# Kernel tuning notes

Hardware: AMD Instinct MI355X
Metric: run time of the kernel (lower is better)

Reference implementation:

```python
import jax, jax.numpy as jnp
import numpy as np

D = 128  # dim_input / kernel_num
S = 1    # support_num
NL, NM, NG = 5, 20, 100

def _norm(x, axis):
    return x / jnp.maximum(jnp.linalg.norm(x, axis=axis, keepdims=True), 1e-12)

def _gather(t, idx):
    # t: (b,n,c), idx: (b,n,k) -> (b,n,k,c)
    return jax.vmap(lambda tb, ib: tb[ib])(t, idx)

def _knn(v, k):
    sq = jnp.sum(v * v, axis=-1)
    d = sq[:, :, None] + sq[:, None, :] - 2.0 * jnp.einsum('bic,bjc->bij', v, v)
    _, idx = jax.lax.top_k(-d, k + 1)
    return idx[:, :, 1:]  # drop self

def _conv_surface(idx, v, dirs):
    nd = _norm(_gather(v, idx) - v[:, :, None, :], -1)                    # (b,n,k,3)
    theta = jax.nn.relu(jnp.einsum('bnkc,cd->bnkd', nd, _norm(dirs, 0)))  # (b,n,k,S*D)
    b, n, k, _ = theta.shape
    theta = theta.reshape(b, n, k, S, D)
    return jnp.sum(jnp.max(theta, axis=2), axis=2)                         # (b,n,D)

def _conv_layer(idx, v, fm, W, bias, dirs):
    nd = _norm(_gather(v, idx) - v[:, :, None, :], -1)
    theta = jax.nn.relu(jnp.einsum('bnkc,cd->bnkd', nd, _norm(dirs, 0)))  # (b,n,k,S*D)
    fo = fm @ W + bias                                                    # (b,n,(S+1)*D)
    fc, fs = fo[..., :D], fo[..., D:]
    fs = _gather(fs, idx)                                                 # (b,n,k,S*D)
    b, n, k, _ = theta.shape
    act = (theta * fs).reshape(b, n, k, S, D)
    return fc + jnp.sum(jnp.max(act, axis=2), axis=2)                     # (b,n,D)

def _bn_relu(x, g, b, eps=1e-5):
    # training-mode BatchNorm1d over (batch, points) per channel, then ReLU
    m = jnp.mean(x, axis=(0, 1))
    v = jnp.var(x, axis=(0, 1))
    return jax.nn.relu((x - m) * jax.lax.rsqrt(v + eps) * g + b)

def setup_inputs() -> dict:
    key = jax.random.key(0)
    ks = jax.random.split(key, 16)
    B, N = 4, 1024
    def u(k, shape, fan):
        s = 1.0 / np.sqrt(fan)
        return jax.random.uniform(k, shape, jnp.float32, -s, s)
    inp = {}
    inp['vertices'] = jax.random.normal(ks[0], (B, N, 3), jnp.float32)
    inp['dirs_l'] = u(ks[1], (3, S * D), S * D)
    inp['dirs_m0'] = u(ks[2], (3, S * D), S * D)
    inp['W_m1'] = u(ks[3], (D, (S + 1) * D), (S + 1) * D)
    inp['b_m1'] = u(ks[4], ((S + 1) * D,), (S + 1) * D)
    inp['dirs_m1'] = u(ks[5], (3, S * D), S * D)
    inp['dirs_g0'] = u(ks[6], (3, S * D), S * D)
    inp['W_g1'] = u(ks[7], (D, (S + 1) * D), (S + 1) * D)
    inp['b_g1'] = u(ks[8], ((S + 1) * D,), (S + 1) * D)
    inp['dirs_g1'] = u(ks[9], (3, S * D), S * D)
    inp['W_g2'] = u(ks[10], (D, (S + 1) * D), (S + 1) * D)
    inp['b_g2'] = u(ks[11], ((S + 1) * D,), (S + 1) * D)
    inp['dirs_g2'] = u(ks[12], (3, S * D), S * D)
    for nm in ['l', 'm0', 'm1', 'g0', 'g1', 'g2']:
        inp['g_' + nm] = jnp.ones((D,), jnp.float32)
        inp['be_' + nm] = jnp.zeros((D,), jnp.float32)
    inp['W_down'] = u(ks[13], (3 * D, 2 * D), 3 * D)
    inp['b_down'] = u(ks[14], (2 * D,), 3 * D)
    return inp

def reference(vertices, dirs_l, dirs_m0, W_m1, b_m1, dirs_m1, dirs_g0, W_g1, b_g1, dirs_g1, W_g2, b_g2, dirs_g2, g_l, be_l, g_m0, be_m0, g_m1, be_m1, g_g0, be_g0, g_g1, be_g1, g_g2, be_g2, W_down, b_down):
    il = _knn(vertices, NL)
    im = _knn(vertices, NM)
    ig = _knn(vertices, NG)
    fm_l = _bn_relu(_conv_surface(il, vertices, dirs_l), g_l, be_l)
    fm_m = _bn_relu(_conv_surface(im, vertices, dirs_m0), g_m0, be_m0)
    fm_m = _bn_relu(_conv_layer(im, vertices, fm_m, W_m1, b_m1, dirs_m1), g_m1, be_m1)
    fm_g = _bn_relu(_conv_surface(ig, vertices, dirs_g0), g_g0, be_g0)
    fm_g = _bn_relu(_conv_layer(ig, vertices, fm_g, W_g1, b_g1, dirs_g1), g_g1, be_g1)
    fm_g = _bn_relu(_conv_layer(ig, vertices, fm_g, W_g2, b_g2, dirs_g2), g_g2, be_g2)
    out = jnp.concatenate((fm_l, fm_m, fm_g), axis=2)                      # (b,n,3D)
    return jax.nn.relu(out @ W_down + b_down)                              # (b,n,2D)
```

## Files before the change

### kernel.cpp

```cpp
#include <hip/hip_runtime.h>
#include <math.h>

typedef unsigned long long u64;

__global__ __launch_bounds__(256) void knnsurf_kernel(
    const float* __restrict__ verts,
    int* __restrict__ idx_out, float4* __restrict__ nd_out,
    const float* __restrict__ dl, const float* __restrict__ dm,
    const float* __restrict__ dg,
    float* __restrict__ raw_l, float* __restrict__ raw_m, float* __restrict__ raw_g)
{
    __shared__ float4 vps[1024];
    __shared__ __align__(16) u64 cand[4][208];
    const int tid = threadIdx.x;
    const int row0 = blockIdx.x * 4;
    const int b = row0 >> 10;
    const float* vb = verts + b * 3072;

    for (int n = tid; n < 1024; n += 256) {
        float x = vb[3 * n], y = vb[3 * n + 1], z = vb[3 * n + 2];
        float s = __fadd_rn(__fadd_rn(__fmul_rn(x, x), __fmul_rn(y, y)),
                            __fmul_rn(z, z));
        vps[n] = make_float4(x, y, z, s);
    }
    __syncthreads();

    const int w = tid >> 6, lane = tid & 63;
    const int row = row0 + w;
    const int n_i = row & 1023;
    const float4 pi = vps[n_i];
    const float xi = pi.x, yi = pi.y, zi = pi.z, sqi = pi.w;

    u64 K[16];
    u64 m1 = ~0ULL, m2 = ~0ULL;
#pragma unroll
    for (int t = 0; t < 16; ++t) {
        int j = t * 64 + lane;
        float4 p = vps[j];
        float dot = __fadd_rn(__fadd_rn(__fmul_rn(xi, p.x),
                                        __fmul_rn(yi, p.y)),
                              __fmul_rn(zi, p.z));
        float d = __fsub_rn(__fadd_rn(sqi, p.w), __fmul_rn(2.0f, dot));
        d = __fadd_rn(d, 0.0f);
        unsigned u = __float_as_uint(d);
        unsigned m = (u & 0x80000000u) ? ~u : (u | 0x80000000u);
        u64 k = ((u64)m << 10) | (unsigned)j;
        K[t] = k;
        bool lt1 = k < m1;
        u64 nm2 = lt1 ? m1 : ((k < m2) ? k : m2);
        m1 = lt1 ? k : m1;
        m2 = nm2;
    }

    u64 tmax = m2, tmin = m1;
#pragma unroll
    for (int off = 1; off < 64; off <<= 1) {
        u64 a = __shfl_xor(tmax, off); if (a > tmax) tmax = a;
        u64 c = __shfl_xor(tmin, off); if (c < tmin) tmin = c;
    }

    u64 T = tmax;
    int chi;
    {
        int c = 0;
#pragma unroll
        for (int t = 0; t < 16; ++t) c += (K[t] < T) ? 1 : 0;
#pragma unroll
        for (int off = 1; off < 64; off <<= 1) c += __shfl_xor(c, off);
        chi = c;
    }
    u64 lo = tmin, hi = T;
    while (chi > 192) {
        u64 mid = (lo + hi) >> 1;
        int c = 0;
#pragma unroll
        for (int t = 0; t < 16; ++t) c += (K[t] < mid) ? 1 : 0;
#pragma unroll
        for (int off = 1; off < 64; off <<= 1) c += __shfl_xor(c, off);
        if (c >= 101) { hi = mid; chi = c; } else lo = mid;
    }
    T = hi;
    const int n = chi;

    int myc_n = 0;
#pragma unroll
    for (int t = 0; t < 16; ++t) myc_n += (K[t] < T) ? 1 : 0;
    int sc = myc_n;
#pragma unroll
    for (int off = 1; off < 64; off <<= 1) {
        int v = __shfl_up(sc, off);
        if (lane >= off) sc += v;
    }
    int pos = sc - myc_n;
#pragma unroll
    for (int t = 0; t < 16; ++t) {
        if (K[t] < T) cand[w][pos++] = K[t];
    }
    if (lane == 0) cand[w][n] = ~0ULL;
    __syncthreads();

    u64 myc[3]; int rk[3];
#pragma unroll
    for (int q = 0; q < 3; ++q) {
        int i = lane + q * 64;
        myc[q] = (i < n) ? cand[w][i] : ~0ULL;
        rk[q] = 0;
    }
    {
        const ulonglong2* c2 = (const ulonglong2*)&cand[w][0];
        const int half = (n + 1) >> 1;
        for (int jj = 0; jj < half; ++jj) {
            ulonglong2 kk = c2[jj];
#pragma unroll
            for (int q = 0; q < 3; ++q) {
                rk[q] += (kk.x < myc[q]) ? 1 : 0;
                rk[q] += (kk.y < myc[q]) ? 1 : 0;
            }
        }
    }

    const int rowbase = row & ~1023;
    float4* nd4w = (float4*)&cand[w][0];
#pragma unroll
    for (int q = 0; q < 3; ++q) {
        int i = lane + q * 64;
        if (i < n) {
            int r = rk[q];
            if (r >= 1 && r <= 100) {
                int slot = r - 1;
                unsigned j = (unsigned)(myc[q] & 1023u);
                idx_out[row * 100 + slot] = rowbase + (int)j;
                float4 pj = vps[j];
                float dx = pj.x - xi, dy = pj.y - yi, dz = pj.z - zi;
                float nrm = sqrtf(__fadd_rn(__fadd_rn(__fmul_rn(dx, dx),
                                                      __fmul_rn(dy, dy)),
                                            __fmul_rn(dz, dz)));
                float inv = 1.0f / fmaxf(nrm, 1e-12f);
                float4 nv = make_float4(dx * inv, dy * inv, dz * inv, 0.0f);
                nd_out[row * 100 + slot] = nv;
                nd4w[slot] = nv;
            }
        }
    }
    __syncthreads();

    const int d = tid & 127;
    float lx = dl[d], ly = dl[128 + d], lz = dl[256 + d];
    float li = 1.0f / fmaxf(sqrtf((lx * lx + ly * ly) + lz * lz), 1e-12f);
    lx *= li; ly *= li; lz *= li;
    float mx = dm[d], my = dm[128 + d], mz = dm[256 + d];
    float mi = 1.0f / fmaxf(sqrtf((mx * mx + my * my) + mz * mz), 1e-12f);
    mx *= mi; my *= mi; mz *= mi;
    float gx = dg[d], gy = dg[128 + d], gz = dg[256 + d];
    float gi = 1.0f / fmaxf(sqrtf((gx * gx + gy * gy) + gz * gz), 1e-12f);
    gx *= gi; gy *= gi; gz *= gi;

#pragma unroll
    for (int p = 0; p < 2; ++p) {
        int rr = (tid >> 7) + 2 * p;
        const float4* ns = (const float4*)&cand[rr][0];
        float ml = -1e30f, mm = -1e30f, mg = -1e30f;
        int k = 0;
        for (; k < 5; ++k) {
            float4 v = ns[k];
            ml = fmaxf(ml, (v.x * lx + v.y * ly) + v.z * lz);
            mm = fmaxf(mm, (v.x * mx + v.y * my) + v.z * mz);
            mg = fmaxf(mg, (v.x * gx + v.y * gy) + v.z * gz);
        }
        for (; k < 20; ++k) {
            float4 v = ns[k];
            mm = fmaxf(mm, (v.x * mx + v.y * my) + v.z * mz);
            mg = fmaxf(mg, (v.x * gx + v.y * gy) + v.z * gz);
        }
        for (; k < 100; ++k) {
            float4 v = ns[k];
            mg = fmaxf(mg, (v.x * gx + v.y * gy) + v.z * gz);
        }
        int orow = row0 + rr;
        raw_l[orow * 128 + d] = fmaxf(ml, 0.0f);
        raw_m[orow * 128 + d] = fmaxf(mm, 0.0f);
        raw_g[orow * 128 + d] = fmaxf(mg, 0.0f);
    }
}

__global__ __launch_bounds__(256) void bnsum_kernel(
    const float* s0, double* p0,
    const float* s1, double* p1,
    const float* s2, double* p2)
{
    const int t = blockIdx.x >> 6;
    const int blk = blockIdx.x & 63;
    const float* src = (t == 0) ? s0 : (t == 1) ? s1 : s2;
    double* p = (t == 0) ? p0 : (t == 1) ? p1 : p2;
    const int tid = threadIdx.x;
    const int c = tid & 127, seg = tid >> 7;
    const float* q = src + ((size_t)blk * 64 + seg * 32) * 128 + c;
    double s = 0.0, ss = 0.0;
    for (int r = 0; r < 32; ++r) { float v = q[r * 128]; s += v; ss += (double)v * v; }
    __shared__ double Ls[2][128], Lq[2][128];
    Ls[seg][c] = s; Lq[seg][c] = ss;
    __syncthreads();
    if (tid < 128) {
        p[blk * 256 + c]       = Ls[0][c] + Ls[1][c];
        p[blk * 256 + 128 + c] = Lq[0][c] + Lq[1][c];
    }
}

__device__ __forceinline__ void compute_st(const double* __restrict__ p,
                                           const float* __restrict__ g,
                                           const float* __restrict__ e,
                                           float* stA, float* stB,
                                           int tid, int nthreads)
{
    for (int c = tid; c < 128; c += nthreads) {
        double S = 0.0, Q = 0.0;
#pragma unroll
        for (int bb = 0; bb < 64; ++bb) { S += p[bb * 256 + c]; Q += p[bb * 256 + 128 + c]; }
        double m = S * (1.0 / 4096.0);
        double var = Q * (1.0 / 4096.0) - m * m;
        double a = (double)g[c] / sqrt(var + 1e-5);
        stA[c] = (float)a;
        stB[c] = (float)((double)e[c] - m * a);
    }
}

__global__ __launch_bounds__(256) void gemm2_kernel(
    const float* __restrict__ Aa, const double* __restrict__ pa,
    const float* __restrict__ ga, const float* __restrict__ ea,
    const float* __restrict__ Wa, const float* __restrict__ ba, float* __restrict__ outa,
    const float* __restrict__ Ab, const double* __restrict__ pb,
    const float* __restrict__ gb, const float* __restrict__ eb,
    const float* __restrict__ Wb, const float* __restrict__ bb, float* __restrict__ outb)
{
    const int job = blockIdx.y;
    const float* A = job ? Ab : Aa;  const double* p = job ? pb : pa;
    const float* g = job ? gb : ga;  const float* e = job ? eb : ea;
    const float* W = job ? Wb : Wa;  const float* bias = job ? bb : ba;
    float* out = job ? outb : outa;

    __shared__ float stA[128], stB[128];
    __shared__ float As[8 * 128];
    const int o = threadIdx.x;
    const int r0 = blockIdx.x * 8;

    compute_st(p, g, e, stA, stB, o, 256);
    __syncthreads();

    for (int t = o; t < 8 * 128; t += 256) {
        int r = t >> 7, c = t & 127;
        As[t] = fmaxf(fmaf(stA[c], A[(r0 + r) * 128 + c], stB[c]), 0.0f);
    }
    __syncthreads();

    float acc[8];
    const float bz = bias[o];
#pragma unroll
    for (int r = 0; r < 8; ++r) acc[r] = bz;

    for (int c = 0; c < 128; c += 4) {
        float w0 = W[(c + 0) * 256 + o];
        float w1 = W[(c + 1) * 256 + o];
        float w2 = W[(c + 2) * 256 + o];
        float w3 = W[(c + 3) * 256 + o];
#pragma unroll
        for (int r = 0; r < 8; ++r) {
            const float4 av = *(const float4*)&As[r * 128 + c];
            acc[r] += av.x * w0 + av.y * w1 + av.z * w2 + av.w * w3;
        }
    }
#pragma unroll
    for (int r = 0; r < 8; ++r)
        out[(r0 + r) * 256 + o] = acc[r];
}

__global__ __launch_bounds__(128) void layer_kernel(
    const float4* __restrict__ nd, const int* __restrict__ idxbuf,
    const float* dir0, const float* fo0, float* out0, int K0,
    const float* dir1, const float* fo1, float* out1, int K1)
{
    const int job = blockIdx.y;
    const float* dirs = job ? dir1 : dir0;
    const float* fo = job ? fo1 : fo0;
    float* out = job ? out1 : out0;
    const int K = job ? K1 : K0;

    const int d = threadIdx.x;
    const int row = blockIdx.x;

    float dx = dirs[d], dy = dirs[128 + d], dz = dirs[256 + d];
    float di = 1.0f / fmaxf(sqrtf((dx * dx + dy * dy) + dz * dz), 1e-12f);
    dx *= di; dy *= di; dz *= di;

    const float4* ns = nd + (size_t)row * 100;
    const int* ib = idxbuf + (size_t)row * 100;

    float acc = -1e30f;
    for (int k4 = 0; k4 < K; k4 += 4) {
        int4 ix4 = *(const int4*)&ib[k4];
        float fs0 = fo[(size_t)ix4.x * 256 + 128 + d];
        float fs1 = fo[(size_t)ix4.y * 256 + 128 + d];
        float fs2 = fo[(size_t)ix4.z * 256 + 128 + d];
        float fs3 = fo[(size_t)ix4.w * 256 + 128 + d];
        float4 v0 = ns[k4 + 0];
        float4 v1 = ns[k4 + 1];
        float4 v2 = ns[k4 + 2];
        float4 v3 = ns[k4 + 3];
        float t0 = fmaxf((v0.x * dx + v0.y * dy) + v0.z * dz, 0.0f);
        float t1 = fmaxf((v1.x * dx + v1.y * dy) + v1.z * dz, 0.0f);
        float t2 = fmaxf((v2.x * dx + v2.y * dy) + v2.z * dz, 0.0f);
        float t3 = fmaxf((v3.x * dx + v3.y * dy) + v3.z * dz, 0.0f);
        acc = fmaxf(acc, t0 * fs0);
        acc = fmaxf(acc, t1 * fs1);
        acc = fmaxf(acc, t2 * fs2);
        acc = fmaxf(acc, t3 * fs3);
    }
    out[row * 128 + d] = fo[row * 256 + d] + acc;
}

__global__ __launch_bounds__(256) void gemmf_kernel(
    const float* __restrict__ A0, const double* __restrict__ p0,
    const float* __restrict__ g0, const float* __restrict__ e0,
    const float* __restrict__ A1, const double* __restrict__ p1,
    const float* __restrict__ g1, const float* __restrict__ e1,
    const float* __restrict__ A2, const double* __restrict__ p2,
    const float* __restrict__ g2, const float* __restrict__ e2,
    const float* __restrict__ W, const float* __restrict__ bias, float* __restrict__ out)
{
    __shared__ float stA[384], stB[384];
    __shared__ float As[8 * 384];
    const int o = threadIdx.x;
    const int r0 = blockIdx.x * 8;

    compute_st(p0, g0, e0, stA,       stB,       o, 256);
    compute_st(p1, g1, e1, stA + 128, stB + 128, o, 256);
    compute_st(p2, g2, e2, stA + 256, stB + 256, o, 256);
    __syncthreads();

    for (int t = o; t < 8 * 384; t += 256) {
        int r = t / 384, c = t - r * 384;
        int seg = c >> 7, cc = c & 127;
        const float* A = (seg == 0) ? A0 : (seg == 1) ? A1 : A2;
        As[t] = fmaxf(fmaf(stA[c], A[(r0 + r) * 128 + cc], stB[c]), 0.0f);
    }
    __syncthreads();

    float acc[8];
    const float bz = bias[o];
#pragma unroll
    for (int r = 0; r < 8; ++r) acc[r] = bz;

    for (int c = 0; c < 384; c += 4) {
        float w0 = W[(c + 0) * 256 + o];
        float w1 = W[(c + 1) * 256 + o];
        float w2 = W[(c + 2) * 256 + o];
        float w3 = W[(c + 3) * 256 + o];
#pragma unroll
        for (int r = 0; r < 8; ++r) {
            const float4 av = *(const float4*)&As[r * 384 + c];
            acc[r] += av.x * w0 + av.y * w1 + av.z * w2 + av.w * w3;
        }
    }
#pragma unroll
    for (int r = 0; r < 8; ++r)
        out[(r0 + r) * 256 + o] = fmaxf(acc[r], 0.0f);
}

extern "C" void kernel_launch(void* const* d_in, const int* in_sizes, int n_in,
                              void* d_out, int out_size, void* d_ws, size_t ws_size,
                              hipStream_t stream)
{
    (void)in_sizes; (void)n_in; (void)out_size; (void)ws_size;

    const float* verts   = (const float*)d_in[0];
    const float* dirs_l  = (const float*)d_in[1];
    const float* dirs_m0 = (const float*)d_in[2];
    const float* W_m1    = (const float*)d_in[3];
    const float* b_m1    = (const float*)d_in[4];
    const float* dirs_m1 = (const float*)d_in[5];
    const float* dirs_g0 = (const float*)d_in[6];
    const float* W_g1    = (const float*)d_in[7];
    const float* b_g1    = (const float*)d_in[8];
    const float* dirs_g1 = (const float*)d_in[9];
    const float* W_g2    = (const float*)d_in[10];
    const float* b_g2    = (const float*)d_in[11];
    const float* dirs_g2 = (const float*)d_in[12];
    const float* g_l  = (const float*)d_in[13]; const float* be_l  = (const float*)d_in[14];
    const float* g_m0 = (const float*)d_in[15]; const float* be_m0 = (const float*)d_in[16];
    const float* g_m1 = (const float*)d_in[17]; const float* be_m1 = (const float*)d_in[18];
    const float* g_g0 = (const float*)d_in[19]; const float* be_g0 = (const float*)d_in[20];
    const float* g_g1 = (const float*)d_in[21]; const float* be_g1 = (const float*)d_in[22];
    const float* g_g2 = (const float*)d_in[23]; const float* be_g2 = (const float*)d_in[24];
    const float* W_down = (const float*)d_in[25];
    const float* b_down = (const float*)d_in[26];

    char* ws = (char*)d_ws;
    const size_t MB = 1 << 20;
    int*    idx100 = (int*)   (ws + 0);
    double* p_l    = (double*)(ws + 2 * MB);
    double* p_m0   = p_l  + 32768;
    double* p_m1   = p_m0 + 32768;
    double* p_g0   = p_m1 + 32768;
    double* p_g1   = p_g0 + 32768;
    double* p_g2   = p_g1 + 32768;
    float4* nd100  = (float4*)(ws + 4 * MB);
    float* raw_l  = (float*)(ws + 11 * MB);
    float* raw_m0 = (float*)(ws + 13 * MB);
    float* raw_g0 = (float*)(ws + 15 * MB);
    float* raw_m1 = (float*)(ws + 17 * MB);
    float* raw_g1 = (float*)(ws + 19 * MB);
    float* raw_g2 = (float*)(ws + 21 * MB);
    float* fo_m   = (float*)(ws + 23 * MB);
    float* fo_g   = (float*)(ws + 27 * MB);
    float* fo_g2  = (float*)(ws + 31 * MB);

    knnsurf_kernel<<<1024, 256, 0, stream>>>(verts, idx100, nd100,
                                             dirs_l, dirs_m0, dirs_g0,
                                             raw_l, raw_m0, raw_g0);
    bnsum_kernel<<<192, 256, 0, stream>>>(raw_l, p_l, raw_m0, p_m0, raw_g0, p_g0);
    gemm2_kernel<<<dim3(512, 2), 256, 0, stream>>>(
        raw_m0, p_m0, g_m0, be_m0, W_m1, b_m1, fo_m,
        raw_g0, p_g0, g_g0, be_g0, W_g1, b_g1, fo_g);
    layer_kernel<<<dim3(4096, 2), 128, 0, stream>>>(nd100, idx100,
                                                    dirs_m1, fo_m, raw_m1, 20,
                                                    dirs_g1, fo_g, raw_g1, 100);
    bnsum_kernel<<<128, 256, 0, stream>>>(raw_m1, p_m1, raw_g1, p_g1, raw_g1, p_g1);
    gemm2_kernel<<<dim3(512, 1), 256, 0, stream>>>(
        raw_g1, p_g1, g_g1, be_g1, W_g2, b_g2, fo_g2,
        raw_g1, p_g1, g_g1, be_g1, W_g2, b_g2, fo_g2);
    layer_kernel<<<dim3(4096, 1), 128, 0, stream>>>(nd100, idx100,
                                                    dirs_g2, fo_g2, raw_g2, 100,
                                                    dirs_g2, fo_g2, raw_g2, 100);
    bnsum_kernel<<<64, 256, 0, stream>>>(raw_g2, p_g2, raw_g2, p_g2, raw_g2, p_g2);
    gemmf_kernel<<<512, 256, 0, stream>>>(raw_l, p_l, g_l, be_l,
                                          raw_m1, p_m1, g_m1, be_m1,
                                          raw_g2, p_g2, g_g2, be_g2,
                                          W_down, b_down, (float*)d_out);
}
```

Baseline: 273.0 us.

## Run dense GEMMs on bf16 MFMA with split-precision hi/lo emulation of fp32

The three dense matmul stages (gemm2 twice, gemmf) move from scalar FP32 FMA loops to MFMA 16x16x32 bf16 instructions. Three products (hi*hi, lo*hi, hi*lo) approximate fp32 accuracy. Weights are pre-split into hi/lo bf16 pairs and reordered into MFMA fragment layout at the tail of the knn kernel, and activations are split the same way into padded LDS. Tiles become 16 rows by 128 columns per block. This targets the ALU cost of the GEMMs, at the price of three MFMAs per tile, some precision loss from the dropped lo*lo term, and extra conversion work in the knn kernel.

```diff
diff --git a/kernel.cpp b/kernel.cpp
--- a/kernel.cpp
+++ b/kernel.cpp
@@ -2,13 +2,54 @@
 #include <math.h>
 
 typedef unsigned long long u64;
+typedef __attribute__((ext_vector_type(8))) short bfrag;
+typedef __attribute__((ext_vector_type(4))) float ffrag;
+
+__device__ __forceinline__ unsigned splitpack(float x)
+{
+    unsigned u = __float_as_uint(x);
+    unsigned hi = u >> 16;
+    float r = x - __uint_as_float(hi << 16);
+    unsigned v = __float_as_uint(r);
+    unsigned lo = (v + 0x7FFFu + ((v >> 16) & 1u)) >> 16;
+    return hi | (lo << 16);
+}
+
+__device__ void conv_wfrag(const float* __restrict__ W, unsigned* __restrict__ dst,
+                           int KB, int gid, int stride)
+{
+    int total = KB * 32 * 256;
+    for (int f = gid; f < total; f += stride) {
+        int i = f & 7;
+        int l = (f >> 3) & 63;
+        int t = f >> 9;
+        int kb = t % KB, ct = t / KB;
+        int k = kb * 32 + (l >> 4) * 8 + i;
+        int n = ct * 16 + (l & 15);
+        dst[f] = splitpack(W[k * 256 + n]);
+    }
+}
+
+#define UNPK8(H, L, q0, q1)                                                         \
+    H[0] = (short)(q0.x); L[0] = (short)(q0.x >> 16);                               \
+    H[1] = (short)(q0.y); L[1] = (short)(q0.y >> 16);                               \
+    H[2] = (short)(q0.z); L[2] = (short)(q0.z >> 16);                               \
+    H[3] = (short)(q0.w); L[3] = (short)(q0.w >> 16);                               \
+    H[4] = (short)(q1.x); L[4] = (short)(q1.x >> 16);                               \
+    H[5] = (short)(q1.y); L[5] = (short)(q1.y >> 16);                               \
+    H[6] = (short)(q1.z); L[6] = (short)(q1.z >> 16);                               \
+    H[7] = (short)(q1.w); L[7] = (short)(q1.w >> 16);
 
 __global__ __launch_bounds__(256) void knnsurf_kernel(
     const float* __restrict__ verts,
     int* __restrict__ idx_out, float4* __restrict__ nd_out,
     const float* __restrict__ dl, const float* __restrict__ dm,
     const float* __restrict__ dg,
-    float* __restrict__ raw_l, float* __restrict__ raw_m, float* __restrict__ raw_g)
+    float* __restrict__ raw_l, float* __restrict__ raw_m, float* __restrict__ raw_g,
+    const float* __restrict__ Wm1, const float* __restrict__ Wg1,
+    const float* __restrict__ Wg2, const float* __restrict__ Wdn,
+    unsigned* __restrict__ wf_m1, unsigned* __restrict__ wf_g1,
+    unsigned* __restrict__ wf_g2, unsigned* __restrict__ wf_dn)
 {
     __shared__ float4 vps[1024];
     __shared__ __align__(16) u64 cand[4][208];
@@ -181,6 +222,14 @@
         raw_m[orow * 128 + d] = fmaxf(mm, 0.0f);
         raw_g[orow * 128 + d] = fmaxf(mg, 0.0f);
     }
+
+    {
+        const int gid = blockIdx.x * 256 + tid;
+        conv_wfrag(Wm1, wf_m1, 4, gid, 262144);
+        conv_wfrag(Wg1, wf_g1, 4, gid, 262144);
+        conv_wfrag(Wg2, wf_g2, 4, gid, 262144);
+        conv_wfrag(Wdn, wf_dn, 12, gid, 262144);
+    }
 }
 
 __global__ __launch_bounds__(256) void bnsum_kernel(
@@ -227,50 +276,71 @@
 __global__ __launch_bounds__(256) void gemm2_kernel(
     const float* __restrict__ Aa, const double* __restrict__ pa,
     const float* __restrict__ ga, const float* __restrict__ ea,
-    const float* __restrict__ Wa, const float* __restrict__ ba, float* __restrict__ outa,
+    const unsigned* __restrict__ Wfa, const float* __restrict__ ba, float* __restrict__ outa,
     const float* __restrict__ Ab, const double* __restrict__ pb,
     const float* __restrict__ gb, const float* __restrict__ eb,
-    const float* __restrict__ Wb, const float* __restrict__ bb, float* __restrict__ outb)
-{
-    const int job = blockIdx.y;
+    const unsigned* __restrict__ Wfb, const float* __restrict__ bb, float* __restrict__ outb)
+{
+    const int job = blockIdx.z;
     const float* A = job ? Ab : Aa;  const double* p = job ? pb : pa;
     const float* g = job ? gb : ga;  const float* e = job ? eb : ea;
-    const float* W = job ? Wb : Wa;  const float* bias = job ? bb : ba;
+    const unsigned* Wf = job ? Wfb : Wfa;
+    const float* bias = job ? bb : ba;
     float* out = job ? outb : outa;
 
     __shared__ float stA[128], stB[128];
-    __shared__ float As[8 * 128];
-    const int o = threadIdx.x;
-    const int r0 = blockIdx.x * 8;
-
-    compute_st(p, g, e, stA, stB, o, 256);
-    __syncthreads();
-
-    for (int t = o; t < 8 * 128; t += 256) {
+    __shared__ __align__(16) unsigned Al[16 * 132];
+    const int tid = threadIdx.x;
+    const int r0 = blockIdx.x * 16;
+
+    compute_st(p, g, e, stA, stB, tid, 256);
+    __syncthreads();
+
+    for (int t = tid; t < 16 * 128; t += 256) {
         int r = t >> 7, c = t & 127;
-        As[t] = fmaxf(fmaf(stA[c], A[(r0 + r) * 128 + c], stB[c]), 0.0f);
-    }
-    __syncthreads();
-
-    float acc[8];
-    const float bz = bias[o];
-#pragma unroll
-    for (int r = 0; r < 8; ++r) acc[r] = bz;
-
-    for (int c = 0; c < 128; c += 4) {
-        float w0 = W[(c + 0) * 256 + o];
-        float w1 = W[(c + 1) * 256 + o];
-        float w2 = W[(c + 2) * 256 + o];
-        float w3 = W[(c + 3) * 256 + o];
-#pragma unroll
-        for (int r = 0; r < 8; ++r) {
-            const float4 av = *(const float4*)&As[r * 128 + c];
-            acc[r] += av.x * w0 + av.y * w1 + av.z * w2 + av.w * w3;
-        }
-    }
-#pragma unroll
-    for (int r = 0; r < 8; ++r)
-        out[(r0 + r) * 256 + o] = acc[r];
+        float v = fmaxf(fmaf(stA[c], A[(size_t)(r0 + r) * 128 + c], stB[c]), 0.0f);
+        Al[r * 132 + c] = splitpack(v);
+    }
+    __syncthreads();
+
+    const int lane = tid & 63, wv = tid >> 6;
+    const int ct0 = blockIdx.y * 8 + wv * 2;
+    const int col0 = ct0 * 16 + (lane & 15);
+    const float bz0 = bias[col0], bz1 = bias[col0 + 16];
+    ffrag acc0 = {bz0, bz0, bz0, bz0};
+    ffrag acc1 = {bz1, bz1, bz1, bz1};
+
+    const unsigned* ap0 = Al + (lane & 15) * 132 + (lane >> 4) * 8;
+
+#pragma unroll
+    for (int kb = 0; kb < 4; ++kb) {
+        const uint4* ap = (const uint4*)(ap0 + kb * 32);
+        uint4 aq0 = ap[0], aq1 = ap[1];
+        bfrag ah, al; UNPK8(ah, al, aq0, aq1)
+        {
+            const uint4* bp = (const uint4*)(Wf + ((size_t)(ct0 * 4 + kb) * 64 + lane) * 8);
+            uint4 bq0 = bp[0], bq1 = bp[1];
+            bfrag bh, bl; UNPK8(bh, bl, bq0, bq1)
+            acc0 = __builtin_amdgcn_mfma_f32_16x16x32_bf16(ah, bh, acc0, 0, 0, 0);
+            acc0 = __builtin_amdgcn_mfma_f32_16x16x32_bf16(al, bh, acc0, 0, 0, 0);
+            acc0 = __builtin_amdgcn_mfma_f32_16x16x32_bf16(ah, bl, acc0, 0, 0, 0);
+        }
+        {
+            const uint4* bp = (const uint4*)(Wf + ((size_t)((ct0 + 1) * 4 + kb) * 64 + lane) * 8);
+            uint4 bq0 = bp[0], bq1 = bp[1];
+            bfrag bh, bl; UNPK8(bh, bl, bq0, bq1)
+            acc1 = __builtin_amdgcn_mfma_f32_16x16x32_bf16(ah, bh, acc1, 0, 0, 0);
+            acc1 = __builtin_amdgcn_mfma_f32_16x16x32_bf16(al, bh, acc1, 0, 0, 0);
+            acc1 = __builtin_amdgcn_mfma_f32_16x16x32_bf16(ah, bl, acc1, 0, 0, 0);
+        }
+    }
+
+    const int rowb = r0 + (lane >> 4) * 4;
+#pragma unroll
+    for (int j = 0; j < 4; ++j) {
+        out[(size_t)(rowb + j) * 256 + col0]      = acc0[j];
+        out[(size_t)(rowb + j) * 256 + col0 + 16] = acc1[j];
+    }
 }
 
 __global__ __launch_bounds__(128) void layer_kernel(
@@ -324,45 +394,66 @@
     const float* __restrict__ g1, const float* __restrict__ e1,
     const float* __restrict__ A2, const double* __restrict__ p2,
     const float* __restrict__ g2, const float* __restrict__ e2,
-    const float* __restrict__ W, const float* __restrict__ bias, float* __restrict__ out)
+    const unsigned* __restrict__ Wf, const float* __restrict__ bias,
+    float* __restrict__ out)
 {
     __shared__ float stA[384], stB[384];
-    __shared__ float As[8 * 384];
-    const int o = threadIdx.x;
-    const int r0 = blockIdx.x * 8;
-
-    compute_st(p0, g0, e0, stA,       stB,       o, 256);
-    compute_st(p1, g1, e1, stA + 128, stB + 128, o, 256);
-    compute_st(p2, g2, e2, stA + 256, stB + 256, o, 256);
-    __syncthreads();
-
-    for (int t = o; t < 8 * 384; t += 256) {
+    __shared__ __align__(16) unsigned Al[16 * 388];
+    const int tid = threadIdx.x;
+    const int r0 = blockIdx.x * 16;
+
+    compute_st(p0, g0, e0, stA,       stB,       tid, 256);
+    compute_st(p1, g1, e1, stA + 128, stB + 128, tid, 256);
+    compute_st(p2, g2, e2, stA + 256, stB + 256, tid, 256);
+    __syncthreads();
+
+    for (int t = tid; t < 16 * 384; t += 256) {
         int r = t / 384, c = t - r * 384;
         int seg = c >> 7, cc = c & 127;
         const float* A = (seg == 0) ? A0 : (seg == 1) ? A1 : A2;
-        As[t] = fmaxf(fmaf(stA[c], A[(r0 + r) * 128 + cc], stB[c]), 0.0f);
-    }
-    __syncthreads();
-
-    float acc[8];
-    const float bz = bias[o];
-#pragma unroll
-    for (int r = 0; r < 8; ++r) acc[r] = bz;
-
-    for (int c = 0; c < 384; c += 4) {
-        float w0 = W[(c + 0) * 256 + o];
-        float w1 = W[(c + 1) * 256 + o];
-        float w2 = W[(c + 2) * 256 + o];
-        float w3 = W[(c + 3) * 256 + o];
-#pragma unroll
-        for (int r = 0; r < 8; ++r) {
-            const float4 av = *(const float4*)&As[r * 384 + c];
-            acc[r] += av.x * w0 + av.y * w1 + av.z * w2 + av.w * w3;
-        }
-    }
-#pragma unroll
-    for (int r = 0; r < 8; ++r)
-        out[(r0 + r) * 256 + o] = fmaxf(acc[r], 0.0f);
+        float v = fmaxf(fmaf(stA[c], A[(size_t)(r0 + r) * 128 + cc], stB[c]), 0.0f);
+        Al[r * 388 + c] = splitpack(v);
+    }
+    __syncthreads();
+
+    const int lane = tid & 63, wv = tid >> 6;
+    const int ct0 = blockIdx.y * 8 + wv * 2;
+    const int col0 = ct0 * 16 + (lane & 15);
+    const float bz0 = bias[col0], bz1 = bias[col0 + 16];
+    ffrag acc0 = {bz0, bz0, bz0, bz0};
+    ffrag acc1 = {bz1, bz1, bz1, bz1};
+
+    const unsigned* ap0 = Al + (lane & 15) * 388 + (lane >> 4) * 8;
+
+#pragma unroll
+    for (int kb = 0; kb < 12; ++kb) {
+        const uint4* ap = (const uint4*)(ap0 + kb * 32);
+        uint4 aq0 = ap[0], aq1 = ap[1];
+        bfrag ah, al; UNPK8(ah, al, aq0, aq1)
+        {
+            const uint4* bp = (const uint4*)(Wf + ((size_t)(ct0 * 12 + kb) * 64 + lane) * 8);
+            uint4 bq0 = bp[0], bq1 = bp[1];
+            bfrag bh, bl; UNPK8(bh, bl, bq0, bq1)
+            acc0 = __builtin_amdgcn_mfma_f32_16x16x32_bf16(ah, bh, acc0, 0, 0, 0);
+            acc0 = __builtin_amdgcn_mfma_f32_16x16x32_bf16(al, bh, acc0, 0, 0, 0);
+            acc0 = __builtin_amdgcn_mfma_f32_16x16x32_bf16(ah, bl, acc0, 0, 0, 0);
+        }
+        {
+            const uint4* bp = (const uint4*)(Wf + ((size_t)((ct0 + 1) * 12 + kb) * 64 + lane) * 8);
+            uint4 bq0 = bp[0], bq1 = bp[1];
+            bfrag bh, bl; UNPK8(bh, bl, bq0, bq1)
+            acc1 = __builtin_amdgcn_mfma_f32_16x16x32_bf16(ah, bh, acc1, 0, 0, 0);
+            acc1 = __builtin_amdgcn_mfma_f32_16x16x32_bf16(al, bh, acc1, 0, 0, 0);
+            acc1 = __builtin_amdgcn_mfma_f32_16x16x32_bf16(ah, bl, acc1, 0, 0, 0);
+        }
+    }
+
+    const int rowb = r0 + (lane >> 4) * 4;
+#pragma unroll
+    for (int j = 0; j < 4; ++j) {
+        out[(size_t)(rowb + j) * 256 + col0]      = fmaxf(acc0[j], 0.0f);
+        out[(size_t)(rowb + j) * 256 + col0 + 16] = fmaxf(acc1[j], 0.0f);
+    }
 }
 
 extern "C" void kernel_launch(void* const* d_in, const int* in_sizes, int n_in,
@@ -412,27 +503,33 @@
     float* fo_m   = (float*)(ws + 23 * MB);
     float* fo_g   = (float*)(ws + 27 * MB);
     float* fo_g2  = (float*)(ws + 31 * MB);
+    unsigned* wf_m1 = (unsigned*)(ws + 36 * MB);
+    unsigned* wf_g1 = (unsigned*)(ws + 37 * MB);
+    unsigned* wf_g2 = (unsigned*)(ws + 38 * MB);
+    unsigned* wf_dn = (unsigned*)(ws + 39 * MB);
 
     knnsurf_kernel<<<1024, 256, 0, stream>>>(verts, idx100, nd100,
                                              dirs_l, dirs_m0, dirs_g0,
-                                             raw_l, raw_m0, raw_g0);
+                                             raw_l, raw_m0, raw_g0,
+                                             W_m1, W_g1, W_g2, W_down,
+                                             wf_m1, wf_g1, wf_g2, wf_dn);
     bnsum_kernel<<<192, 256, 0, stream>>>(raw_l, p_l, raw_m0, p_m0, raw_g0, p_g0);
-    gemm2_kernel<<<dim3(512, 2), 256, 0, stream>>>(
-        raw_m0, p_m0, g_m0, be_m0, W_m1, b_m1, fo_m,
-        raw_g0, p_g0, g_g0, be_g0, W_g1, b_g1, fo_g);
+    gemm2_kernel<<<dim3(256, 2, 2), 256, 0, stream>>>(
+        raw_m0, p_m0, g_m0, be_m0, wf_m1, b_m1, fo_m,
+        raw_g0, p_g0, g_g0, be_g0, wf_g1, b_g1, fo_g);
     layer_kernel<<<dim3(4096, 2), 128, 0, stream>>>(nd100, idx100,
                                                     dirs_m1, fo_m, raw_m1, 20,
                                                     dirs_g1, fo_g, raw_g1, 100);
     bnsum_kernel<<<128, 256, 0, stream>>>(raw_m1, p_m1, raw_g1, p_g1, raw_g1, p_g1);
-    gemm2_kernel<<<dim3(512, 1), 256, 0, stream>>>(
-        raw_g1, p_g1, g_g1, be_g1, W_g2, b_g2, fo_g2,
-        raw_g1, p_g1, g_g1, be_g1, W_g2, b_g2, fo_g2);
+    gemm2_kernel<<<dim3(256, 2, 1), 256, 0, stream>>>(
+        raw_g1, p_g1, g_g1, be_g1, wf_g2, b_g2, fo_g2,
+        raw_g1, p_g1, g_g1, be_g1, wf_g2, b_g2, fo_g2);
     layer_kernel<<<dim3(4096, 1), 128, 0, stream>>>(nd100, idx100,
                                                     dirs_g2, fo_g2, raw_g2, 100,
                                                     dirs_g2, fo_g2, raw_g2, 100);
     bnsum_kernel<<<64, 256, 0, stream>>>(raw_g2, p_g2, raw_g2, p_g2, raw_g2, p_g2);
-    gemmf_kernel<<<512, 256, 0, stream>>>(raw_l, p_l, g_l, be_l,
-                                          raw_m1, p_m1, g_m1, be_m1,
-                                          raw_g2, p_g2, g_g2, be_g2,
-                                          W_down, b_down, (float*)d_out);
-}
+    gemmf_kernel<<<dim3(256, 2), 256, 0, stream>>>(raw_l, p_l, g_l, be_l,
+                                                   raw_m1, p_m1, g_m1, be_m1,
+                                                   raw_g2, p_g2, g_g2, be_g2,
+                                                   wf_dn, b_down, (float*)d_out);
+}
```

Result: faster. 238.8 us, median of 3 (-12.5%).
